# Performance work log

Measured on AMD Instinct MI355X. Metric: run time of the kernel, lower is better.

Reference implementation:

```python
import jax, jax.numpy as jnp
import numpy as np

B, S, D, H = 2, 2048, 2048, 16
DH = D // H  # 128 head dim
ROPE_THETA = 10000.0
LN_EPS = 1e-5


def setup_inputs() -> dict:
    key = jax.random.key(0)
    k1, k2, k3 = jax.random.split(key, 3)
    positions = jnp.broadcast_to(jnp.arange(S, dtype=jnp.int64), (B, S))
    hidden_states = jax.random.normal(k1, (B, S, D), dtype=jnp.float32)
    w_qkv = jax.random.normal(k2, (D, 3 * D), dtype=jnp.float32) * 0.02
    w_out = jax.random.normal(k3, (D, D), dtype=jnp.float32) * 0.02
    return {"positions": positions, "hidden_states": hidden_states,
            "w_qkv": w_qkv, "w_out": w_out}


def _rope(x, positions):
    # NeoX-style rotary (vLLM get_rope default): rotate split halves.
    # x: [B, S, H, DH], positions: [B, S]
    half = DH // 2
    inv_freq = 1.0 / (ROPE_THETA ** (jnp.arange(0, half, dtype=jnp.float32) / half))
    ang = positions.astype(jnp.float32)[..., None] * inv_freq  # [B, S, half]
    cos = jnp.cos(ang)[:, :, None, :]  # [B, S, 1, half]
    sin = jnp.sin(ang)[:, :, None, :]
    x1, x2 = x[..., :half], x[..., half:]
    return jnp.concatenate([x1 * cos - x2 * sin, x2 * cos + x1 * sin], axis=-1)


def reference(positions, hidden_states, w_qkv, w_out):
    # LayerNorm with no affine params (elementwise_affine=False)
    mu = jnp.mean(hidden_states, axis=-1, keepdims=True)
    var = jnp.mean(jnp.square(hidden_states - mu), axis=-1, keepdims=True)
    x = (hidden_states - mu) * jax.lax.rsqrt(var + LN_EPS)

    qkv = jnp.einsum('bsd,de->bse', x, w_qkv)  # [B, S, 3D]
    q, k, v = jnp.split(qkv, 3, axis=-1)
    q = q.reshape(B, S, H, DH)
    k = k.reshape(B, S, H, DH)
    v = v.reshape(B, S, H, DH)

    q = _rope(q, positions)
    k = _rope(k, positions)

    scale = DH ** -0.5
    scores = jnp.einsum('bqhd,bkhd->bhqk', q, k) * scale  # [B, H, S, S]
    causal = jnp.tril(jnp.ones((S, S), dtype=bool))
    scores = jnp.where(causal, scores, jnp.finfo(scores.dtype).min)
    probs = jax.nn.softmax(scores, axis=-1)
    attn = jnp.einsum('bhqk,bkhd->bqhd', probs, v).reshape(B, S, D)

    return jnp.einsum('bsd,de->bse', attn, w_out)
```

## Files before the change

kernel.cpp:

```cpp
#include <hip/hip_runtime.h>


typedef __bf16 bf16x8 __attribute__((ext_vector_type(8)));
typedef float f32x4 __attribute__((ext_vector_type(4)));

__device__ __forceinline__ unsigned short f2bf(float f) {
  unsigned u = __builtin_bit_cast(unsigned, f);
  u = u + 0x7fffu + ((u >> 16) & 1u);
  return (unsigned short)(u >> 16);
}
__device__ __forceinline__ float bf2f(unsigned short h) {
  unsigned u = ((unsigned)h) << 16;
  return __builtin_bit_cast(float, u);
}

#define GLD_LDS16(gp, lp)                                                      \
  __builtin_amdgcn_global_load_lds((__attribute__((address_space(1))) void*)(gp), \
                                   (__attribute__((address_space(3))) void*)(lp), \
                                   16, 0, 0)

__global__ __launch_bounds__(256) void ln_kernel(const float* __restrict__ hs,
                                                 unsigned short* __restrict__ xb) {
  const int row = blockIdx.x;
  const int tid = threadIdx.x;
  const float* rp = hs + (size_t)row * 2048;
  const float4 v0 = ((const float4*)rp)[tid];
  const float4 v1 = ((const float4*)rp)[tid + 256];
  float s  = v0.x + v0.y + v0.z + v0.w + v1.x + v1.y + v1.z + v1.w;
  float ss = v0.x*v0.x + v0.y*v0.y + v0.z*v0.z + v0.w*v0.w
           + v1.x*v1.x + v1.y*v1.y + v1.z*v1.z + v1.w*v1.w;
#pragma unroll
  for (int m = 1; m < 64; m <<= 1) { s += __shfl_xor(s, m); ss += __shfl_xor(ss, m); }
  __shared__ float rs[4], rss[4];
  if ((tid & 63) == 0) { rs[tid >> 6] = s; rss[tid >> 6] = ss; }
  __syncthreads();
  s  = rs[0] + rs[1] + rs[2] + rs[3];
  ss = rss[0] + rss[1] + rss[2] + rss[3];
  const float mean = s * (1.0f / 2048.0f);
  const float var  = ss * (1.0f / 2048.0f) - mean * mean;
  const float inv  = rsqrtf(var + 1e-5f);
  ushort4 o0, o1;
  o0.x = f2bf((v0.x - mean) * inv); o0.y = f2bf((v0.y - mean) * inv);
  o0.z = f2bf((v0.z - mean) * inv); o0.w = f2bf((v0.w - mean) * inv);
  o1.x = f2bf((v1.x - mean) * inv); o1.y = f2bf((v1.y - mean) * inv);
  o1.z = f2bf((v1.z - mean) * inv); o1.w = f2bf((v1.w - mean) * inv);
  ushort4* op = (ushort4*)(xb + (size_t)row * 2048);
  op[tid] = o0; op[tid + 256] = o1;
}

__global__ __launch_bounds__(256) void cast_transpose2(const float* __restrict__ wqkv,
                                                       const float* __restrict__ wout,
                                                       unsigned short* __restrict__ wqkvT,
                                                       unsigned short* __restrict__ woutT) {
  __shared__ float t[32][33];
  const int bx = blockIdx.x;
  const float* in;
  unsigned short* out;
  int N, n0;
  if (bx < 192) { in = wqkv; out = wqkvT; N = 6144; n0 = bx * 32; }
  else          { in = wout; out = woutT; N = 2048; n0 = (bx - 192) * 32; }
  const int k0 = blockIdx.y * 32;
  const int tx = threadIdx.x, ty = threadIdx.y;
#pragma unroll
  for (int i = 0; i < 4; i++)
    t[ty + i * 8][tx] = in[(size_t)(k0 + ty + i * 8) * N + n0 + tx];
  __syncthreads();
#pragma unroll
  for (int i = 0; i < 4; i++)
    out[(size_t)(n0 + ty + i * 8) * 2048 + k0 + tx] = f2bf(t[tx][ty + i * 8]);
}

template <int OUT_BF16>
__global__ __launch_bounds__(256) void gemm_bt(const unsigned short* __restrict__ A,
                                               const unsigned short* __restrict__ Bt,
                                               void* __restrict__ Cv,
                                               int M, int N, int K) {
  __shared__ alignas(16) unsigned short sA[128 * 64];
  __shared__ alignas(16) unsigned short sB[128 * 64];
  const int tid = threadIdx.x;
  const int lane = tid & 63, wave = tid >> 6;
  const int wm = wave >> 1, wn = wave & 1;
  const int ln15 = lane & 15, quad = lane >> 4;
  const size_t m0 = (size_t)blockIdx.y * 128, n0 = (size_t)blockIdx.x * 128;
  const unsigned short* Ag = A + m0 * (size_t)K;
  const unsigned short* Bg = Bt + n0 * (size_t)K;
  const int lr8 = lane >> 3;
  const int sc8 = ((lane & 7) ^ (lr8 & 7)) * 8;
  const int xk = ln15 & 7;

  f32x4 acc[4][4];
#pragma unroll
  for (int mi = 0; mi < 4; mi++)
#pragma unroll
    for (int ni = 0; ni < 4; ni++) acc[mi][ni] = (f32x4){0.f, 0.f, 0.f, 0.f};

  const int iters = K >> 6;
  for (int kt = 0; kt < iters; ++kt) {
    const int kb = kt * 64;
    __syncthreads();
#pragma unroll
    for (int i = 0; i < 4; i++) {
      const int c = wave * 4 + i;
      const int row = c * 8 + lr8;
      GLD_LDS16(Ag + (size_t)row * K + kb + sc8, &sA[c * 512]);
      GLD_LDS16(Bg + (size_t)row * K + kb + sc8, &sB[c * 512]);
    }
    __syncthreads();
#pragma unroll
    for (int ks = 0; ks < 2; ks++) {
      bf16x8 af[4], bf[4];
#pragma unroll
      for (int mi = 0; mi < 4; mi++)
        af[mi] = *(const bf16x8*)&sA[(wm * 64 + mi * 16 + ln15) * 64 +
                                     ((ks * 4 + quad) ^ xk) * 8];
#pragma unroll
      for (int ni = 0; ni < 4; ni++)
        bf[ni] = *(const bf16x8*)&sB[(wn * 64 + ni * 16 + ln15) * 64 +
                                     ((ks * 4 + quad) ^ xk) * 8];
#pragma unroll
      for (int mi = 0; mi < 4; mi++)
#pragma unroll
        for (int ni = 0; ni < 4; ni++)
          acc[mi][ni] = __builtin_amdgcn_mfma_f32_16x16x32_bf16(af[mi], bf[ni], acc[mi][ni], 0, 0, 0);
    }
  }
#pragma unroll
  for (int mi = 0; mi < 4; mi++)
#pragma unroll
    for (int ni = 0; ni < 4; ni++) {
      const size_t col = n0 + wn * 64 + ni * 16 + ln15;
#pragma unroll
      for (int r = 0; r < 4; r++) {
        const size_t row = m0 + wm * 64 + mi * 16 + quad * 4 + r;
        if (OUT_BF16)
          ((unsigned short*)Cv)[row * N + col] = f2bf(acc[mi][ni][r]);
        else
          ((float*)Cv)[row * N + col] = acc[mi][ni][r];
      }
    }
}

__global__ __launch_bounds__(256) void rope_kernel(const unsigned short* __restrict__ qkv,
                                                   unsigned short* __restrict__ Qo,
                                                   unsigned short* __restrict__ Ko) {
  const int t = blockIdx.x * 256 + threadIdx.x;
  const int g = t & 7;
  const int h = (t >> 3) & 15;
  const int row = t >> 7;
  const int s = row & 2047;
  const size_t base = (size_t)row * 6144 + h * 128 + g * 8;
  const bf16x8 q1 = *(const bf16x8*)&qkv[base];
  const bf16x8 q2 = *(const bf16x8*)&qkv[base + 64];
  const bf16x8 k1 = *(const bf16x8*)&qkv[base + 2048];
  const bf16x8 k2 = *(const bf16x8*)&qkv[base + 2048 + 64];
  const float qscale = 0.08838834764831845f;
  bf16x8 oq1, oq2, ok1, ok2;
#pragma unroll
  for (int j = 0; j < 8; j++) {
    const int i = g * 8 + j;
    const float freq = exp2f(-(float)i * (13.287712379549449f / 64.0f));
    float rev = (float)s * freq * 0.15915494309189535f;
    rev -= floorf(rev);
    const float ar = rev * 6.283185307179586f;
    const float sn = __sinf(ar), cs = __cosf(ar);
    const float a1 = (float)q1[j], a2 = (float)q2[j];
    const float b1 = (float)k1[j], b2 = (float)k2[j];
    oq1[j] = (__bf16)((a1 * cs - a2 * sn) * qscale);
    oq2[j] = (__bf16)((a2 * cs + a1 * sn) * qscale);
    ok1[j] = (__bf16)(b1 * cs - b2 * sn);
    ok2[j] = (__bf16)(b2 * cs + b1 * sn);
  }
  const size_t ob = ((size_t)(((row >> 11) << 4) + h) * 2048 + s) * 128 + g * 8;
  *(bf16x8*)&Qo[ob]      = oq1;
  *(bf16x8*)&Qo[ob + 64] = oq2;
  *(bf16x8*)&Ko[ob]      = ok1;
  *(bf16x8*)&Ko[ob + 64] = ok2;
}

__global__ __launch_bounds__(256) void vtrans_kernel(const unsigned short* __restrict__ qkv,
                                                     unsigned short* __restrict__ VT) {
  __shared__ unsigned short t[32][34];
  const int s0 = blockIdx.x * 32, d0 = blockIdx.y * 32;
  const int bh = blockIdx.z, b = bh >> 4, h = bh & 15;
  const int tx = threadIdx.x, ty = threadIdx.y;
#pragma unroll
  for (int i = 0; i < 4; i++)
    t[ty + i * 8][tx] =
        qkv[(size_t)(b * 2048 + s0 + ty + i * 8) * 6144 + 4096 + h * 128 + d0 + tx];
  __syncthreads();
#pragma unroll
  for (int i = 0; i < 4; i++)
    VT[((size_t)bh * 128 + d0 + ty + i * 8) * 2048 + s0 + tx] = t[tx][ty + i * 8];
}

__global__ __launch_bounds__(256) void flash_kernel(const unsigned short* __restrict__ Q,
                                                    const unsigned short* __restrict__ Kbuf,
                                                    const unsigned short* __restrict__ VT,
                                                    unsigned short* __restrict__ attn) {
  __shared__ alignas(16) unsigned short sK[64 * 128];
  __shared__ alignas(16) unsigned short sVT[128 * 64];
  __shared__ alignas(16) unsigned short sP[64 * 72];

  const int bh = blockIdx.y;
  const int b = bh >> 4, h = bh & 15;
  const int tid = threadIdx.x;
  const int lane = tid & 63, w = tid >> 6;
  const int ln15 = lane & 15, quad = lane >> 4;

  const unsigned short* Qg = Q + (size_t)bh * 2048 * 128;
  const unsigned short* Kg = Kbuf + (size_t)bh * 2048 * 128;
  const unsigned short* Vg = VT + (size_t)bh * 128 * 2048;

  const float L2E = 1.44269504088896f;
  bf16x8 onesf;
#pragma unroll
  for (int j = 0; j < 8; j++) onesf[j] = (__bf16)1.0f;

#pragma unroll 1
  for (int t = 0; t < 2; t++) {
    const int qt = t ? (31 - (int)blockIdx.x) : (int)blockIdx.x;
    const int q0 = qt * 64;

    bf16x8 qf[4];
#pragma unroll
    for (int ks = 0; ks < 4; ks++)
      qf[ks] = *(const bf16x8*)&Qg[(size_t)(q0 + w * 16 + ln15) * 128 + ks * 32 + quad * 8];

    f32x4 o[8], ol;
#pragma unroll
    for (int nd = 0; nd < 8; nd++) o[nd] = (f32x4){0.f, 0.f, 0.f, 0.f};
    ol = (f32x4){0.f, 0.f, 0.f, 0.f};
    float mrow[4];
#pragma unroll
    for (int r = 0; r < 4; r++) mrow[r] = -1e30f;

#pragma unroll 1
    for (int j = 0; j <= qt; j++) {
      const int k0 = j * 64;
      __syncthreads();
#pragma unroll
      for (int i = 0; i < 4; i++) {
        const int c = w * 4 + i;
        const int row = c * 4 + (lane >> 4);
        const int ch = (lane & 15) ^ (row & 15);
        GLD_LDS16(Kg + (size_t)(k0 + row) * 128 + ch * 8, &sK[c * 512]);
      }
#pragma unroll
      for (int i = 0; i < 4; i++) {
        const int c = w * 4 + i;
        const int row = c * 8 + (lane >> 3);
        const int ch = (lane & 7) ^ (row & 7);
        GLD_LDS16(Vg + (size_t)row * 2048 + k0 + ch * 8, &sVT[c * 512]);
      }
      __syncthreads();

      f32x4 sc[4];
#pragma unroll
      for (int ni = 0; ni < 4; ni++) sc[ni] = (f32x4){0.f, 0.f, 0.f, 0.f};
#pragma unroll
      for (int ks = 0; ks < 4; ks++) {
        bf16x8 bk[4];
#pragma unroll
        for (int ni = 0; ni < 4; ni++) {
          const int row = ni * 16 + ln15;
          const int ch = (ks * 4 + quad) ^ (row & 15);
          bk[ni] = *(const bf16x8*)&sK[row * 128 + ch * 8];
        }
#pragma unroll
        for (int ni = 0; ni < 4; ni++)
          sc[ni] = __builtin_amdgcn_mfma_f32_16x16x32_bf16(qf[ks], bk[ni], sc[ni], 0, 0, 0);
      }

      float mt[4] = {-1e30f, -1e30f, -1e30f, -1e30f};
      if (j == qt) {
#pragma unroll
        for (int ni = 0; ni < 4; ni++) {
          const int key = k0 + ni * 16 + ln15;
#pragma unroll
          for (int r = 0; r < 4; r++) {
            const int qrow = q0 + w * 16 + quad * 4 + r;
            float v = sc[ni][r];
            if (key > qrow) v = -1e30f;
            sc[ni][r] = v;
            mt[r] = fmaxf(mt[r], v);
          }
        }
      } else {
#pragma unroll
        for (int ni = 0; ni < 4; ni++)
#pragma unroll
          for (int r = 0; r < 4; r++) mt[r] = fmaxf(mt[r], sc[ni][r]);
      }
#pragma unroll
      for (int r = 0; r < 4; r++) {
        float m = mt[r];
        m = fmaxf(m, __shfl_xor(m, 1));
        m = fmaxf(m, __shfl_xor(m, 2));
        m = fmaxf(m, __shfl_xor(m, 4));
        m = fmaxf(m, __shfl_xor(m, 8));
        const float mnew = fmaxf(mrow[r], m);
        const float alpha = exp2f((mrow[r] - mnew) * L2E);
        mrow[r] = mnew;
#pragma unroll
        for (int ni = 0; ni < 4; ni++)
          sc[ni][r] = exp2f((sc[ni][r] - mnew) * L2E);
        ol[r] *= alpha;
#pragma unroll
        for (int nd = 0; nd < 8; nd++) o[nd][r] *= alpha;
      }
#pragma unroll
      for (int ni = 0; ni < 4; ni++)
#pragma unroll
        for (int r = 0; r < 4; r++)
          sP[(w * 16 + quad * 4 + r) * 72 + ni * 16 + ln15] = f2bf(sc[ni][r]);

      bf16x8 pf[2];
#pragma unroll
      for (int kk = 0; kk < 2; kk++)
        pf[kk] = *(const bf16x8*)&sP[(w * 16 + ln15) * 72 + kk * 32 + quad * 8];
#pragma unroll
      for (int kk = 0; kk < 2; kk++) {
#pragma unroll
        for (int nd = 0; nd < 8; nd++) {
          const int row = nd * 16 + ln15;
          const int ch = (kk * 4 + quad) ^ (row & 7);
          const bf16x8 bv = *(const bf16x8*)&sVT[row * 64 + ch * 8];
          o[nd] = __builtin_amdgcn_mfma_f32_16x16x32_bf16(pf[kk], bv, o[nd], 0, 0, 0);
        }
        ol = __builtin_amdgcn_mfma_f32_16x16x32_bf16(pf[kk], onesf, ol, 0, 0, 0);
      }
    }

#pragma unroll
    for (int r = 0; r < 4; r++) {
      const float inv = 1.0f / ol[r];
      const int qrow = q0 + w * 16 + quad * 4 + r;
#pragma unroll
      for (int nd = 0; nd < 8; nd++) {
        const int d = nd * 16 + ln15;
        attn[((size_t)(b * 2048 + qrow)) * 2048 + h * 128 + d] = f2bf(o[nd][r] * inv);
      }
    }
  }
}

extern "C" void kernel_launch(void* const* d_in, const int* in_sizes, int n_in,
                              void* d_out, int out_size, void* d_ws, size_t ws_size,
                              hipStream_t stream) {
  const float* hs   = (const float*)d_in[1];
  const float* wqkv = (const float*)d_in[2];
  const float* wout = (const float*)d_in[3];
  float* out = (float*)d_out;
  char* ws = (char*)d_ws;

  unsigned short* x_bf  = (unsigned short*)(ws);
  unsigned short* wqkvT = (unsigned short*)(ws + 16777216);
  unsigned short* woutT = (unsigned short*)(ws + 41943040);
  unsigned short* qkv   = (unsigned short*)(ws + 50331648);
  unsigned short* Qb    = (unsigned short*)(ws + 100663296);
  unsigned short* Kb    = (unsigned short*)(ws + 117440512);
  unsigned short* VT    = wqkvT;
  unsigned short* attn  = x_bf;

  ln_kernel<<<4096, 256, 0, stream>>>(hs, x_bf);
  cast_transpose2<<<dim3(256, 64), dim3(32, 8), 0, stream>>>(wqkv, wout, wqkvT, woutT);
  gemm_bt<1><<<dim3(48, 32), 256, 0, stream>>>(x_bf, wqkvT, (void*)qkv, 4096, 6144, 2048);
  rope_kernel<<<2048, 256, 0, stream>>>(qkv, Qb, Kb);
  vtrans_kernel<<<dim3(64, 4, 32), dim3(32, 8), 0, stream>>>(qkv, VT);
  flash_kernel<<<dim3(16, 32), 256, 0, stream>>>(Qb, Kb, VT, attn);
  gemm_bt<0><<<dim3(16, 32), 256, 0, stream>>>(attn, woutT, (void*)out, 4096, 2048, 2048);
}
```

Before: 424.7 us.

## Double-buffer K/V tiles in flash attention and merge small prep kernels

The flash attention loop now keeps two LDS buffers for the K and V^T tiles. It prefetches the next tile with async global-to-LDS loads while computing on the current one, instead of loading and waiting before each tile. Separately, layernorm and the weight cast-transpose are merged into one launch, and RoPE and the V transpose into another, which cuts launch count. Double buffering raises LDS usage per block, which may lower occupancy. It also depends on the single barrier per iteration being enough to order the async loads against the reads.

After: 421.2 us. No clear change (-0.8%).

```diff
diff --git a/kernel.cpp b/kernel.cpp
--- a/kernel.cpp
+++ b/kernel.cpp
@@ -19,48 +19,50 @@
                                    (__attribute__((address_space(3))) void*)(lp), \
                                    16, 0, 0)
 
-__global__ __launch_bounds__(256) void ln_kernel(const float* __restrict__ hs,
-                                                 unsigned short* __restrict__ xb) {
-  const int row = blockIdx.x;
+__global__ __launch_bounds__(256) void prep_kernel(const float* __restrict__ hs,
+                                                   const float* __restrict__ wqkv,
+                                                   const float* __restrict__ wout,
+                                                   unsigned short* __restrict__ xb,
+                                                   unsigned short* __restrict__ wqkvT,
+                                                   unsigned short* __restrict__ woutT) {
   const int tid = threadIdx.x;
-  const float* rp = hs + (size_t)row * 2048;
-  const float4 v0 = ((const float4*)rp)[tid];
-  const float4 v1 = ((const float4*)rp)[tid + 256];
-  float s  = v0.x + v0.y + v0.z + v0.w + v1.x + v1.y + v1.z + v1.w;
-  float ss = v0.x*v0.x + v0.y*v0.y + v0.z*v0.z + v0.w*v0.w
-           + v1.x*v1.x + v1.y*v1.y + v1.z*v1.z + v1.w*v1.w;
-#pragma unroll
-  for (int m = 1; m < 64; m <<= 1) { s += __shfl_xor(s, m); ss += __shfl_xor(ss, m); }
-  __shared__ float rs[4], rss[4];
-  if ((tid & 63) == 0) { rs[tid >> 6] = s; rss[tid >> 6] = ss; }
-  __syncthreads();
-  s  = rs[0] + rs[1] + rs[2] + rs[3];
-  ss = rss[0] + rss[1] + rss[2] + rss[3];
-  const float mean = s * (1.0f / 2048.0f);
-  const float var  = ss * (1.0f / 2048.0f) - mean * mean;
-  const float inv  = rsqrtf(var + 1e-5f);
-  ushort4 o0, o1;
-  o0.x = f2bf((v0.x - mean) * inv); o0.y = f2bf((v0.y - mean) * inv);
-  o0.z = f2bf((v0.z - mean) * inv); o0.w = f2bf((v0.w - mean) * inv);
-  o1.x = f2bf((v1.x - mean) * inv); o1.y = f2bf((v1.y - mean) * inv);
-  o1.z = f2bf((v1.z - mean) * inv); o1.w = f2bf((v1.w - mean) * inv);
-  ushort4* op = (ushort4*)(xb + (size_t)row * 2048);
-  op[tid] = o0; op[tid + 256] = o1;
-}
-
-__global__ __launch_bounds__(256) void cast_transpose2(const float* __restrict__ wqkv,
-                                                       const float* __restrict__ wout,
-                                                       unsigned short* __restrict__ wqkvT,
-                                                       unsigned short* __restrict__ woutT) {
-  __shared__ float t[32][33];
-  const int bx = blockIdx.x;
+  int bx = blockIdx.x;
+  if (bx < 4096) {
+    const float* rp = hs + (size_t)bx * 2048;
+    const float4 v0 = ((const float4*)rp)[tid];
+    const float4 v1 = ((const float4*)rp)[tid + 256];
+    float s  = v0.x + v0.y + v0.z + v0.w + v1.x + v1.y + v1.z + v1.w;
+    float ss = v0.x*v0.x + v0.y*v0.y + v0.z*v0.z + v0.w*v0.w
+             + v1.x*v1.x + v1.y*v1.y + v1.z*v1.z + v1.w*v1.w;
+#pragma unroll
+    for (int m = 1; m < 64; m <<= 1) { s += __shfl_xor(s, m); ss += __shfl_xor(ss, m); }
+    __shared__ float rs[4], rss[4];
+    if ((tid & 63) == 0) { rs[tid >> 6] = s; rss[tid >> 6] = ss; }
+    __syncthreads();
+    s  = rs[0] + rs[1] + rs[2] + rs[3];
+    ss = rss[0] + rss[1] + rss[2] + rss[3];
+    const float mean = s * (1.0f / 2048.0f);
+    const float var  = ss * (1.0f / 2048.0f) - mean * mean;
+    const float inv  = rsqrtf(var + 1e-5f);
+    ushort4 o0, o1;
+    o0.x = f2bf((v0.x - mean) * inv); o0.y = f2bf((v0.y - mean) * inv);
+    o0.z = f2bf((v0.z - mean) * inv); o0.w = f2bf((v0.w - mean) * inv);
+    o1.x = f2bf((v1.x - mean) * inv); o1.y = f2bf((v1.y - mean) * inv);
+    o1.z = f2bf((v1.z - mean) * inv); o1.w = f2bf((v1.w - mean) * inv);
+    ushort4* op = (ushort4*)(xb + (size_t)bx * 2048);
+    op[tid] = o0; op[tid + 256] = o1;
+    return;
+  }
+  bx -= 4096;
+  const int bxx = bx & 255, byy = bx >> 8;
   const float* in;
   unsigned short* out;
   int N, n0;
-  if (bx < 192) { in = wqkv; out = wqkvT; N = 6144; n0 = bx * 32; }
-  else          { in = wout; out = woutT; N = 2048; n0 = (bx - 192) * 32; }
-  const int k0 = blockIdx.y * 32;
-  const int tx = threadIdx.x, ty = threadIdx.y;
+  if (bxx < 192) { in = wqkv; out = wqkvT; N = 6144; n0 = bxx * 32; }
+  else           { in = wout; out = woutT; N = 2048; n0 = (bxx - 192) * 32; }
+  const int k0 = byy * 32;
+  const int tx = tid & 31, ty = tid >> 5;
+  __shared__ float t[32][33];
 #pragma unroll
   for (int i = 0; i < 4; i++)
     t[ty + i * 8][tx] = in[(size_t)(k0 + ty + i * 8) * N + n0 + tx];
@@ -140,49 +142,53 @@
     }
 }
 
-__global__ __launch_bounds__(256) void rope_kernel(const unsigned short* __restrict__ qkv,
-                                                   unsigned short* __restrict__ Qo,
-                                                   unsigned short* __restrict__ Ko) {
-  const int t = blockIdx.x * 256 + threadIdx.x;
-  const int g = t & 7;
-  const int h = (t >> 3) & 15;
-  const int row = t >> 7;
-  const int s = row & 2047;
-  const size_t base = (size_t)row * 6144 + h * 128 + g * 8;
-  const bf16x8 q1 = *(const bf16x8*)&qkv[base];
-  const bf16x8 q2 = *(const bf16x8*)&qkv[base + 64];
-  const bf16x8 k1 = *(const bf16x8*)&qkv[base + 2048];
-  const bf16x8 k2 = *(const bf16x8*)&qkv[base + 2048 + 64];
-  const float qscale = 0.08838834764831845f;
-  bf16x8 oq1, oq2, ok1, ok2;
-#pragma unroll
-  for (int j = 0; j < 8; j++) {
-    const int i = g * 8 + j;
-    const float freq = exp2f(-(float)i * (13.287712379549449f / 64.0f));
-    float rev = (float)s * freq * 0.15915494309189535f;
-    rev -= floorf(rev);
-    const float ar = rev * 6.283185307179586f;
-    const float sn = __sinf(ar), cs = __cosf(ar);
-    const float a1 = (float)q1[j], a2 = (float)q2[j];
-    const float b1 = (float)k1[j], b2 = (float)k2[j];
-    oq1[j] = (__bf16)((a1 * cs - a2 * sn) * qscale);
-    oq2[j] = (__bf16)((a2 * cs + a1 * sn) * qscale);
-    ok1[j] = (__bf16)(b1 * cs - b2 * sn);
-    ok2[j] = (__bf16)(b2 * cs + b1 * sn);
+__global__ __launch_bounds__(256) void rv_kernel(const unsigned short* __restrict__ qkv,
+                                                 unsigned short* __restrict__ Qo,
+                                                 unsigned short* __restrict__ Ko,
+                                                 unsigned short* __restrict__ VT) {
+  const int tid = threadIdx.x;
+  const int bx = blockIdx.x;
+  if (bx < 2048) {
+    const int t = bx * 256 + tid;
+    const int g = t & 7;
+    const int h = (t >> 3) & 15;
+    const int row = t >> 7;
+    const int s = row & 2047;
+    const size_t base = (size_t)row * 6144 + h * 128 + g * 8;
+    const bf16x8 q1 = *(const bf16x8*)&qkv[base];
+    const bf16x8 q2 = *(const bf16x8*)&qkv[base + 64];
+    const bf16x8 k1 = *(const bf16x8*)&qkv[base + 2048];
+    const bf16x8 k2 = *(const bf16x8*)&qkv[base + 2048 + 64];
+    const float qscale = 0.08838834764831845f;
+    bf16x8 oq1, oq2, ok1, ok2;
+#pragma unroll
+    for (int j = 0; j < 8; j++) {
+      const int i = g * 8 + j;
+      const float freq = exp2f(-(float)i * (13.287712379549449f / 64.0f));
+      float rev = (float)s * freq * 0.15915494309189535f;
+      rev -= floorf(rev);
+      const float ar = rev * 6.283185307179586f;
+      const float sn = __sinf(ar), cs = __cosf(ar);
+      const float a1 = (float)q1[j], a2 = (float)q2[j];
+      const float b1 = (float)k1[j], b2 = (float)k2[j];
+      oq1[j] = (__bf16)((a1 * cs - a2 * sn) * qscale);
+      oq2[j] = (__bf16)((a2 * cs + a1 * sn) * qscale);
+      ok1[j] = (__bf16)(b1 * cs - b2 * sn);
+      ok2[j] = (__bf16)(b2 * cs + b1 * sn);
+    }
+    const size_t ob = ((size_t)(((row >> 11) << 4) + h) * 2048 + s) * 128 + g * 8;
+    *(bf16x8*)&Qo[ob]      = oq1;
+    *(bf16x8*)&Qo[ob + 64] = oq2;
+    *(bf16x8*)&Ko[ob]      = ok1;
+    *(bf16x8*)&Ko[ob + 64] = ok2;
+    return;
   }
-  const size_t ob = ((size_t)(((row >> 11) << 4) + h) * 2048 + s) * 128 + g * 8;
-  *(bf16x8*)&Qo[ob]      = oq1;
-  *(bf16x8*)&Qo[ob + 64] = oq2;
-  *(bf16x8*)&Ko[ob]      = ok1;
-  *(bf16x8*)&Ko[ob + 64] = ok2;
-}
-
-__global__ __launch_bounds__(256) void vtrans_kernel(const unsigned short* __restrict__ qkv,
-                                                     unsigned short* __restrict__ VT) {
+  const int idx = bx - 2048;
+  const int s0 = (idx & 63) * 32;
+  const int d0 = ((idx >> 6) & 3) * 32;
+  const int bh = idx >> 8, b = bh >> 4, h = bh & 15;
+  const int tx = tid & 31, ty = tid >> 5;
   __shared__ unsigned short t[32][34];
-  const int s0 = blockIdx.x * 32, d0 = blockIdx.y * 32;
-  const int bh = blockIdx.z, b = bh >> 4, h = bh & 15;
-  const int tx = threadIdx.x, ty = threadIdx.y;
 #pragma unroll
   for (int i = 0; i < 4; i++)
     t[ty + i * 8][tx] =
@@ -197,8 +203,8 @@
                                                     const unsigned short* __restrict__ Kbuf,
                                                     const unsigned short* __restrict__ VT,
                                                     unsigned short* __restrict__ attn) {
-  __shared__ alignas(16) unsigned short sK[64 * 128];
-  __shared__ alignas(16) unsigned short sVT[128 * 64];
+  __shared__ alignas(16) unsigned short sK[2][64 * 128];
+  __shared__ alignas(16) unsigned short sVT[2][128 * 64];
   __shared__ alignas(16) unsigned short sP[64 * 72];
 
   const int bh = blockIdx.y;
@@ -216,6 +222,11 @@
 #pragma unroll
   for (int j = 0; j < 8; j++) onesf[j] = (__bf16)1.0f;
 
+  const int kcrow = (lane >> 4);
+  const int kch = (lane & 15);
+  const int vcrow = (lane >> 3);
+  const int vch = (lane & 7);
+
 #pragma unroll 1
   for (int t = 0; t < 2; t++) {
     const int qt = t ? (31 - (int)blockIdx.x) : (int)blockIdx.x;
@@ -234,25 +245,40 @@
 #pragma unroll
     for (int r = 0; r < 4; r++) mrow[r] = -1e30f;
 
+    __syncthreads();
+#pragma unroll
+    for (int i = 0; i < 4; i++) {
+      const int c = w * 4 + i;
+      const int row = c * 4 + kcrow;
+      GLD_LDS16(Kg + (size_t)row * 128 + (kch ^ (row & 15)) * 8, &sK[0][c * 512]);
+    }
+#pragma unroll
+    for (int i = 0; i < 4; i++) {
+      const int c = w * 4 + i;
+      const int row = c * 8 + vcrow;
+      GLD_LDS16(Vg + (size_t)row * 2048 + (vch ^ (row & 7)) * 8, &sVT[0][c * 512]);
+    }
+
 #pragma unroll 1
     for (int j = 0; j <= qt; j++) {
-      const int k0 = j * 64;
+      const int cur = j & 1;
       __syncthreads();
-#pragma unroll
-      for (int i = 0; i < 4; i++) {
-        const int c = w * 4 + i;
-        const int row = c * 4 + (lane >> 4);
-        const int ch = (lane & 15) ^ (row & 15);
-        GLD_LDS16(Kg + (size_t)(k0 + row) * 128 + ch * 8, &sK[c * 512]);
-      }
-#pragma unroll
-      for (int i = 0; i < 4; i++) {
-        const int c = w * 4 + i;
-        const int row = c * 8 + (lane >> 3);
-        const int ch = (lane & 7) ^ (row & 7);
-        GLD_LDS16(Vg + (size_t)row * 2048 + k0 + ch * 8, &sVT[c * 512]);
-      }
-      __syncthreads();
+      if (j < qt) {
+        const int k0n = (j + 1) * 64;
+        const int nxt = cur ^ 1;
+#pragma unroll
+        for (int i = 0; i < 4; i++) {
+          const int c = w * 4 + i;
+          const int row = c * 4 + kcrow;
+          GLD_LDS16(Kg + (size_t)(k0n + row) * 128 + (kch ^ (row & 15)) * 8, &sK[nxt][c * 512]);
+        }
+#pragma unroll
+        for (int i = 0; i < 4; i++) {
+          const int c = w * 4 + i;
+          const int row = c * 8 + vcrow;
+          GLD_LDS16(Vg + (size_t)row * 2048 + k0n + (vch ^ (row & 7)) * 8, &sVT[nxt][c * 512]);
+        }
+      }
 
       f32x4 sc[4];
 #pragma unroll
@@ -264,7 +290,7 @@
         for (int ni = 0; ni < 4; ni++) {
           const int row = ni * 16 + ln15;
           const int ch = (ks * 4 + quad) ^ (row & 15);
-          bk[ni] = *(const bf16x8*)&sK[row * 128 + ch * 8];
+          bk[ni] = *(const bf16x8*)&sK[cur][row * 128 + ch * 8];
         }
 #pragma unroll
         for (int ni = 0; ni < 4; ni++)
@@ -273,6 +299,7 @@
 
       float mt[4] = {-1e30f, -1e30f, -1e30f, -1e30f};
       if (j == qt) {
+        const int k0 = j * 64;
 #pragma unroll
         for (int ni = 0; ni < 4; ni++) {
           const int key = k0 + ni * 16 + ln15;
@@ -324,7 +351,7 @@
         for (int nd = 0; nd < 8; nd++) {
           const int row = nd * 16 + ln15;
           const int ch = (kk * 4 + quad) ^ (row & 7);
-          const bf16x8 bv = *(const bf16x8*)&sVT[row * 64 + ch * 8];
+          const bf16x8 bv = *(const bf16x8*)&sVT[cur][row * 64 + ch * 8];
           o[nd] = __builtin_amdgcn_mfma_f32_16x16x32_bf16(pf[kk], bv, o[nd], 0, 0, 0);
         }
         ol = __builtin_amdgcn_mfma_f32_16x16x32_bf16(pf[kk], onesf, ol, 0, 0, 0);
@@ -362,11 +389,9 @@
   unsigned short* VT    = wqkvT;
   unsigned short* attn  = x_bf;
 
-  ln_kernel<<<4096, 256, 0, stream>>>(hs, x_bf);
-  cast_transpose2<<<dim3(256, 64), dim3(32, 8), 0, stream>>>(wqkv, wout, wqkvT, woutT);
+  prep_kernel<<<4096 + 16384, 256, 0, stream>>>(hs, wqkv, wout, x_bf, wqkvT, woutT);
   gemm_bt<1><<<dim3(48, 32), 256, 0, stream>>>(x_bf, wqkvT, (void*)qkv, 4096, 6144, 2048);
-  rope_kernel<<<2048, 256, 0, stream>>>(qkv, Qb, Kb);
-  vtrans_kernel<<<dim3(64, 4, 32), dim3(32, 8), 0, stream>>>(qkv, VT);
+  rv_kernel<<<2048 + 8192, 256, 0, stream>>>(qkv, Qb, Kb, VT);
   flash_kernel<<<dim3(16, 32), 256, 0, stream>>>(Qb, Kb, VT, attn);
   gemm_bt<0><<<dim3(16, 32), 256, 0, stream>>>(attn, woutT, (void*)out, 4096, 2048, 2048);
 }
```
